# Kernel tuning notes

Measured on AMD Instinct MI355X. Metric: run time of the kernel, lower is better.

Reference implementation:

```python
import jax, jax.numpy as jnp
import numpy as np
from jax import lax

EMBED_DIM = 128
HIDDEN = 50
KS = 7
BN_EPS = 1e-5


def setup_inputs() -> dict:
    key = jax.random.key(0)
    ks = jax.random.split(key, 8)
    B, L, D, H = 4, 512, EMBED_DIM, HIDDEN
    x1 = jax.random.normal(ks[0], (B, L, D), jnp.float32)
    x2 = jax.random.normal(ks[1], (B, L, D), jnp.float32)
    # conv1 (1x1) weight stored as [H, 2D] (spatial dims of size 1 dropped)
    conv1_w = jax.random.normal(ks[2], (H, 2 * D), jnp.float32) * (1.0 / np.sqrt(2 * D))
    conv1_b = jnp.zeros((H,), jnp.float32)
    bn1_g = jnp.ones((H,), jnp.float32)
    bn1_b = jnp.zeros((H,), jnp.float32)
    w2 = jax.random.normal(ks[3], (1, H, KS, KS), jnp.float32) * (1.0 / np.sqrt(H * KS * KS))
    conv2_w = 0.5 * (w2 + jnp.swapaxes(w2, 2, 3))  # clip(): symmetrize kernel
    conv2_b = jnp.zeros((1,), jnp.float32)
    bn2_g = jnp.ones((1,), jnp.float32)
    bn2_b = jnp.zeros((1,), jnp.float32)
    return {"x1": x1, "x2": x2, "conv1_w": conv1_w, "conv1_b": conv1_b,
            "bn1_g": bn1_g, "bn1_b": bn1_b, "conv2_w": conv2_w, "conv2_b": conv2_b,
            "bn2_g": bn2_g, "bn2_b": bn2_b}


def _batch_norm(x, g, b):
    # train-mode BN: batch statistics over (N, H, W), biased variance (PyTorch)
    m = jnp.mean(x, axis=(0, 2, 3), keepdims=True)
    v = jnp.var(x, axis=(0, 2, 3), keepdims=True)
    xn = (x - m) * lax.rsqrt(v + BN_EPS)
    return xn * g[None, :, None, None] + b[None, :, None, None]


def reference(x1, x2, conv1_w, conv1_b, bn1_g, bn1_b, conv2_w, conv2_b, bn2_g, bn2_b):
    # x1, x2: [B, L, D] -> channel-first [B, D, L]
    x1c = jnp.swapaxes(x1, 1, 2)
    x2c = jnp.swapaxes(x2, 1, 2)
    D = x1c.shape[1]
    w_dif, w_mul = conv1_w[:, :D], conv1_w[:, D:]
    # 1x1 conv over concat([|x1_i - x2_j|, x1_i * x2_j]) fused as two contractions
    dif = jnp.abs(x1c[:, :, :, None] - x2c[:, :, None, :])        # [B, D, L1, L2]
    h = jnp.einsum('bdij,hd->bhij', dif, w_dif)
    h = h + jnp.einsum('bdi,bdj,hd->bhij', x1c, x2c, w_mul)       # mul term, no [B,D,L,L] materialized by hand
    h = h + conv1_b[None, :, None, None]
    h = jax.nn.relu(h)                 # activation1 BEFORE batch_norm1 (as in source)
    h = _batch_norm(h, bn1_g, bn1_b)
    # conv2: symmetric 7x7, padding ks//2 == SAME for odd ks
    y = lax.conv_general_dilated(h, conv2_w, window_strides=(1, 1), padding='SAME',
                                 dimension_numbers=('NCHW', 'OIHW', 'NCHW'))
    y = y + conv2_b[None, :, None, None]
    y = _batch_norm(y, bn2_g, bn2_b)
    y = jax.nn.sigmoid(y)
    return y[:, 0, :, :]               # squeeze channel -> [B, L1, L2]
```

## Files before the change

kernel.cpp:

```cpp
#include <hip/hip_runtime.h>

#define LL 512
#define DD 128
#define HH 50
#define JW 520

typedef short v8s __attribute__((ext_vector_type(8)));
typedef float f32x4 __attribute__((ext_vector_type(4)));
typedef unsigned int u32x4 __attribute__((ext_vector_type(4)));

__device__ __forceinline__ unsigned cvtpk(float a, float b) {
  unsigned r;
  asm("v_cvt_pk_bf16_f32 %0, %1, %2" : "=v"(r) : "v"(a), "v"(b));
  return r;
}
__device__ __forceinline__ unsigned cvtpkabs(float a, float b) {
  unsigned r;
  asm("v_cvt_pk_bf16_f32 %0, abs(%1), abs(%2)" : "=v"(r) : "v"(a), "v"(b));
  return r;
}
__device__ __forceinline__ unsigned short f2bf(float f) {
  unsigned u = __builtin_bit_cast(unsigned, f);
  u = (u + 0x7fffu + ((u >> 16) & 1u)) >> 16;
  return (unsigned short)u;
}
__device__ __forceinline__ void gload_lds16(const unsigned short* g, unsigned short* l) {
  __builtin_amdgcn_global_load_lds(
      (const __attribute__((address_space(1))) unsigned int*)g,
      (__attribute__((address_space(3))) unsigned int*)l, 16, 0, 0);
}

__global__ __launch_bounds__(256, 2) void pass1(
    const float* __restrict__ x1, const float* __restrict__ x2,
    const float* __restrict__ c1w, const float* __restrict__ c1b,
    unsigned short* __restrict__ hbuf, float* __restrict__ partials)
{
  __shared__ float x1s[32][128];
  __shared__ unsigned short wgt[64][264];
  __shared__ float stred[4][128];

  const int tid = threadIdx.x;
  const int wv = tid >> 6, lane = tid & 63;
  const int lh = lane & 15, lg = lane >> 4;
  const int bx = blockIdx.x, by = blockIdx.y, bz = blockIdx.z;
  const int j0 = bx << 6, i0 = by << 5;

  {
    int r = tid >> 3, c = (tid & 7) << 4;
    const float* g = x1 + ((size_t)(bz * LL + i0 + r) * DD + c);
#pragma unroll
    for (int u = 0; u < 4; ++u)
      *(f32x4*)&x1s[r][c + 4 * u] = *(const f32x4*)(g + 4 * u);
  }
  {
#pragma unroll
    for (int it = 0; it < 16; ++it) {
      int flat = (it * 256 + tid) << 2;
      int h = flat >> 8, col = flat & 255;
      f32x4 v = (h < HH) ? *(const f32x4*)(c1w + flat) : f32x4{0.f, 0.f, 0.f, 0.f};
      unsigned lo = cvtpk(v[0], v[1]), hi = cvtpk(v[2], v[3]);
      *(unsigned long long*)&wgt[h][col] = ((unsigned long long)hi << 32) | lo;
    }
  }
  __syncthreads();

  v8s bfr[4][8];
  {
    const unsigned wbase = (unsigned)(size_t)
        ((__attribute__((address_space(3))) char*)&wgt[0][0]);
#pragma unroll
    for (int n = 0; n < 4; n++)
#pragma unroll
      for (int kt = 0; kt < 8; kt++) {
        unsigned off = wbase + (unsigned)(((n * 16 + lh) * 264 + kt * 32 + lg * 8) << 1);
        asm volatile("ds_read_b128 %0, %1" : "=v"(bfr[n][kt]) : "v"(off));
      }
    asm volatile("s_waitcnt lgkmcnt(0)" ::: "memory");
    __builtin_amdgcn_sched_barrier(0);
  }

  float x2v[4][8];
  {
    const int j = j0 + (wv << 4) + lh;
    const float* g = x2 + ((size_t)(bz * LL + j) * DD + (lg << 3));
#pragma unroll
    for (int kt = 0; kt < 4; kt++) {
      f32x4 a = *(const f32x4*)(g + kt * 32);
      f32x4 b = *(const f32x4*)(g + kt * 32 + 4);
#pragma unroll
      for (int e = 0; e < 4; e++) { x2v[kt][e] = a[e]; x2v[kt][4 + e] = b[e]; }
    }
  }
  float bias[4][4];
#pragma unroll
  for (int n = 0; n < 4; n++)
#pragma unroll
    for (int q = 0; q < 4; q++) {
      int h = n * 16 + (lg << 2) + q;
      bias[n][q] = (h < HH) ? c1b[h] : 0.f;
    }

  float ssum[4][4], ssq[4][4];
#pragma unroll
  for (int n = 0; n < 4; n++)
#pragma unroll
    for (int q = 0; q < 4; q++) { ssum[n][q] = 0.f; ssq[n][q] = 0.f; }

  unsigned short* hb = hbuf +
      ((size_t)(bz * LL + i0) * JW + 4 + j0 + (wv << 4) + lh) * 64 + (lg << 2);

#pragma unroll 2
  for (int di = 0; di < 32; ++di) {
    f32x4 acc[4];
#pragma unroll
    for (int n = 0; n < 4; n++) acc[n] = f32x4{0.f, 0.f, 0.f, 0.f};
#pragma unroll
    for (int kt = 0; kt < 4; ++kt) {
      f32x4 p = *(const f32x4*)&x1s[di][kt * 32 + (lg << 3)];
      f32x4 r = *(const f32x4*)&x1s[di][kt * 32 + (lg << 3) + 4];
      float xv[8];
#pragma unroll
      for (int e = 0; e < 4; e++) { xv[e] = p[e]; xv[4 + e] = r[e]; }
      u32x4 ad, am;
#pragma unroll
      for (int m = 0; m < 4; m++) {
        ad[m] = cvtpkabs(xv[2*m] - x2v[kt][2*m], xv[2*m+1] - x2v[kt][2*m+1]);
        am[m] = cvtpk(xv[2*m] * x2v[kt][2*m], xv[2*m+1] * x2v[kt][2*m+1]);
      }
      v8s vad = __builtin_bit_cast(v8s, ad);
      v8s vam = __builtin_bit_cast(v8s, am);
#pragma unroll
      for (int n = 0; n < 4; n++)
        acc[n] = __builtin_amdgcn_mfma_f32_16x16x32_bf16(bfr[n][kt], vad, acc[n], 0, 0, 0);
#pragma unroll
      for (int n = 0; n < 4; n++)
        acc[n] = __builtin_amdgcn_mfma_f32_16x16x32_bf16(bfr[n][kt + 4], vam, acc[n], 0, 0, 0);
    }
    unsigned short* hp = hb + (size_t)di * (JW * 64);
#pragma unroll
    for (int n = 0; n < 4; ++n) {
      float vv[4];
#pragma unroll
      for (int q = 0; q < 4; ++q) {
        float v = acc[n][q] + bias[n][q];
        v = fmaxf(v, 0.f);
        ssum[n][q] += v; ssq[n][q] += v * v;
        vv[q] = v;
      }
      unsigned lo = cvtpk(vv[0], vv[1]), hi = cvtpk(vv[2], vv[3]);
      *(unsigned long long*)(hp + n * 16) = ((unsigned long long)hi << 32) | lo;
    }
  }

#pragma unroll
  for (int n = 0; n < 4; ++n)
#pragma unroll
    for (int q = 0; q < 4; ++q) {
      float s = ssum[n][q], t = ssq[n][q];
#pragma unroll
      for (int m = 1; m < 16; m <<= 1) { s += __shfl_xor(s, m); t += __shfl_xor(t, m); }
      if (lh == 0) {
        stred[wv][n * 16 + (lg << 2) + q] = s;
        stred[wv][64 + n * 16 + (lg << 2) + q] = t;
      }
    }
  __syncthreads();
  if (tid < 128) {
    int bid = (bz * gridDim.y + by) * gridDim.x + bx;
    partials[bid * 128 + tid] = stred[0][tid] + stred[1][tid] + stred[2][tid] + stred[3][tid];
  }

  if (bx == 0 || bx == 7) {
    const int jb = (bx == 0) ? 0 : 516;
#pragma unroll
    for (int k = 0; k < 4; ++k) {
      int unit = tid + (k << 8);
      int ii = unit >> 5;
      int rem = unit & 31;
      int jj = jb + (rem >> 3);
      int ch = (rem & 7) << 3;
      u32x4 z = {0u, 0u, 0u, 0u};
      *(u32x4*)&hbuf[((size_t)(bz * LL + i0 + ii) * JW + jj) * 64 + ch] = z;
    }
  }
}

__global__ void pass2a(const float* __restrict__ partials, float* __restrict__ red1)
{
  __shared__ float acc2[2][128];
  const int tid = threadIdx.x, b = blockIdx.x;
  const int slot = tid & 127, half = tid >> 7;
  float s = 0.f;
#pragma unroll
  for (int k = 0; k < 4; k++)
    s += partials[(b * 8 + half * 4 + k) * 128 + slot];
  acc2[half][slot] = s;
  __syncthreads();
  if (tid < 128) red1[b * 128 + tid] = acc2[0][tid] + acc2[1][tid];
}

__global__ void pass2b(const float* __restrict__ red1,
                       const float* __restrict__ c2w, const float* __restrict__ c2b,
                       const float* __restrict__ bn1g, const float* __restrict__ bn1b,
                       unsigned short* __restrict__ wA, float* __restrict__ tmap)
{
  __shared__ float acc2[2][128];
  __shared__ float sq[128];
  __shared__ float aa[64], cc[64];
  __shared__ float wlds[2450];
  __shared__ float tpart[49][5];
  const int tid = threadIdx.x;
  const int slot = tid & 127, half = tid >> 7;
  float s = 0.f;
#pragma unroll
  for (int k = 0; k < 32; k++) s += red1[(half * 32 + k) * 128 + slot];
  acc2[half][slot] = s;
  __syncthreads();
  if (tid < 128) sq[tid] = acc2[0][tid] + acc2[1][tid];
  for (int i = tid; i < 2450; i += 256) wlds[i] = c2w[i];
  __syncthreads();
  if (tid < HH) {
    float S = sq[tid], Q = sq[64 + tid];
    const float N = 4.0f * 512.f * 512.f;
    float m = S / N, v = fmaxf(Q / N - m * m, 0.f);
    float a = bn1g[tid] * rsqrtf(v + 1e-5f);
    aa[tid] = a;
    cc[tid] = bn1b[tid] - m * a;
  }
  __syncthreads();
  for (int idx = tid; idx < 16 * 448; idx += 256) {
    int ky = idx / 448, r = idx - ky * 448;
    int kx = r >> 6, ch = r & 63;
    float v = (ky < 7 && ch < HH) ? aa[ch] * wlds[ch * 49 + ky * 7 + kx] : 0.f;
    wA[idx] = f2bf(v);
  }
  if (tid < 245) {
    int c = tid / 5, g = tid - (tid / 5) * 5;
    int ci = c / 7, cj = c - (c / 7) * 7;
    int kylo = ci < 3 ? 3 - ci : 0, kyhi = ci > 3 ? 9 - ci : 6;
    int kxlo = cj < 3 ? 3 - cj : 0, kxhi = cj > 3 ? 9 - cj : 6;
    float t = 0.f;
    for (int h = g * 10; h < g * 10 + 10; h++) {
      float sm = 0.f;
      for (int ky = kylo; ky <= kyhi; ky++)
        for (int kx = kxlo; kx <= kxhi; kx++) sm += wlds[h * 49 + ky * 7 + kx];
      t += cc[h] * sm;
    }
    tpart[c][g] = t;
  }
  __syncthreads();
  if (tid < 49)
    tmap[tid] = c2b[0] + tpart[tid][0] + tpart[tid][1] + tpart[tid][2]
              + tpart[tid][3] + tpart[tid][4];
}

__global__ __launch_bounds__(256, 4) void pass3(
    const unsigned short* __restrict__ hbuf, const unsigned short* __restrict__ wA,
    const float* __restrict__ tmap, float* __restrict__ ybuf, float* __restrict__ part2)
{
  __shared__ unsigned short T[2][72 * 64];
  __shared__ float tm[49];
  __shared__ float rs[4], rq[4];

  const int tid = threadIdx.x;
  const int wv = tid >> 6, lane = tid & 63;
  const int lh = lane & 15, lg = lane >> 4;
  const int bx = blockIdx.x, by = blockIdx.y, bz = blockIdx.z;
  const int j0 = bx << 6, i0 = by << 4;

  v8s afr[14];
#pragma unroll
  for (int kt = 0; kt < 14; kt++)
    afr[kt] = *(const v8s*)&wA[lh * 448 + kt * 32 + (lg << 3)];

  if (tid < 49) tm[tid] = tmap[tid];

  const int jc = (wv << 4) + lh;
  float ya[4] = {0.f, 0.f, 0.f, 0.f};

  auto stage = [&](int buf, int row) {
    const unsigned short* rowp = hbuf + ((size_t)(bz * LL + row) * JW + j0) * 64;
#pragma unroll
    for (int cc2 = 0; cc2 < 2; ++cc2) {
      const int c = wv + (cc2 << 2);
      const int u = (c << 6) + lane;
      const int tj = u >> 3, oct = u & 7;
      gload_lds16(rowp + tj * 64 + ((oct ^ (tj & 7)) << 3), &T[buf][c << 9]);
    }
    if (wv == 0) {
      const int u = 512 + lane;
      const int tj = u >> 3, oct = u & 7;
      gload_lds16(rowp + tj * 64 + ((oct ^ (tj & 7)) << 3), &T[buf][8 << 9]);
    }
  };

  { const int r0 = i0 - 3; if (r0 >= 0) stage(0, r0); }
  __syncthreads();

  for (int rb = 0; rb < 24; rb += 8) {
#pragma unroll
    for (int u8 = 0; u8 < 8; ++u8) {
      const int rr = rb + u8;
      const int r = i0 - 3 + rr;
      const int cur = rr & 1;
      if (rr + 1 < 22) {
        const int rn = r + 1;
        if (rn >= 0 && rn < LL) stage(cur ^ 1, rn);
      }
      if (rr < 22 && r >= 0 && r < LL) {
        f32x4 a0 = {0.f, 0.f, 0.f, 0.f}, a1 = {0.f, 0.f, 0.f, 0.f};
#pragma unroll
        for (int kt = 0; kt < 14; ++kt) {
          const int kx = kt >> 1;
          const int t = jc + 1 + kx;
          const int sl = ((kt & 1) << 2) + lg;
          v8s b = *(const v8s*)&T[cur][(t << 6) + ((sl ^ (t & 7)) << 3)];
          if (kt & 1) a1 = __builtin_amdgcn_mfma_f32_16x16x32_bf16(afr[kt], b, a1, 0, 0, 0);
          else        a0 = __builtin_amdgcn_mfma_f32_16x16x32_bf16(afr[kt], b, a0, 0, 0, 0);
        }
        float zq[4];
#pragma unroll
        for (int q = 0; q < 4; ++q) zq[q] = a0[q] + a1[q];
#pragma unroll
        for (int ky = 0; ky < 7; ++ky) {
          float zz = __shfl(zq[ky & 3], ((ky >> 2) << 4) + lh, 64);
          const int idx = rr - ky;
          const bool ok = ((unsigned)idx < 16u) && ((idx >> 2) == lg);
          ya[(u8 - ky) & 3] += ok ? zz : 0.f;
        }
      }
      __syncthreads();
    }
  }

  float sa = 0.f, qa = 0.f;
  const int jj = j0 + jc;
  const int cj = jj < 3 ? jj : (jj > 508 ? jj - 505 : 3);
#pragma unroll
  for (int s = 0; s < 4; ++s) {
    const int i = i0 + (lg << 2) + s;
    const int ci = i < 3 ? i : (i > 508 ? i - 505 : 3);
    float v = ya[s] + tm[ci * 7 + cj];
    ybuf[(size_t)(bz * LL + i) * LL + jj] = v;
    sa += v; qa += v * v;
  }
#pragma unroll
  for (int m = 1; m < 64; m <<= 1) { sa += __shfl_xor(sa, m); qa += __shfl_xor(qa, m); }
  if (lane == 0) { rs[wv] = sa; rq[wv] = qa; }
  __syncthreads();
  if (tid == 0) {
    const int bid = (bz * gridDim.y + by) * gridDim.x + bx;
    part2[bid] = rs[0] + rs[1] + rs[2] + rs[3];
    part2[1024 + bid] = rq[0] + rq[1] + rq[2] + rq[3];
  }
}

__global__ void pass3b(const float* __restrict__ part2, float* __restrict__ stats2)
{
  __shared__ float rs[4], rq[4];
  const int tid = threadIdx.x;
  float s = 0.f, q = 0.f;
  for (int i = tid; i < 1024; i += 256) { s += part2[i]; q += part2[1024 + i]; }
#pragma unroll
  for (int m = 1; m < 64; m <<= 1) { s += __shfl_xor(s, m); q += __shfl_xor(q, m); }
  const int wave = tid >> 6, lane = tid & 63;
  if (lane == 0) { rs[wave] = s; rq[wave] = q; }
  __syncthreads();
  if (tid == 0) {
    float S = rs[0] + rs[1] + rs[2] + rs[3];
    float Q = rq[0] + rq[1] + rq[2] + rq[3];
    const float N = 4.0f * 512.f * 512.f;
    float m2 = S / N, v2 = fmaxf(Q / N - m2 * m2, 0.f);
    stats2[0] = m2;
    stats2[1] = rsqrtf(v2 + 1e-5f);
  }
}

__global__ void pass4(const float* __restrict__ y, const float* __restrict__ stats2,
                      const float* __restrict__ bn2g, const float* __restrict__ bn2b,
                      float* __restrict__ out)
{
  const int idx = blockIdx.x * 256 + threadIdx.x;
  const float m2 = stats2[0], inv = stats2[1];
  const float g = bn2g[0], b = bn2b[0];
  f32x4 v = ((const f32x4*)y)[idx];
  f32x4 r;
#pragma unroll
  for (int e = 0; e < 4; e++) {
    float xn = (v[e] - m2) * inv * g + b;
    r[e] = 1.f / (1.f + __expf(-xn));
  }
  ((f32x4*)out)[idx] = r;
}

extern "C" void kernel_launch(void* const* d_in, const int* in_sizes, int n_in,
                              void* d_out, int out_size, void* d_ws, size_t ws_size,
                              hipStream_t stream) {
  (void)in_sizes; (void)n_in; (void)out_size; (void)ws_size;
  const float* x1   = (const float*)d_in[0];
  const float* x2   = (const float*)d_in[1];
  const float* c1w  = (const float*)d_in[2];
  const float* c1b  = (const float*)d_in[3];
  const float* bn1g = (const float*)d_in[4];
  const float* bn1b = (const float*)d_in[5];
  const float* c2w  = (const float*)d_in[6];
  const float* c2b  = (const float*)d_in[7];
  const float* bn2g = (const float*)d_in[8];
  const float* bn2b = (const float*)d_in[9];

  char* ws = (char*)d_ws;
  float* partials       = (float*)(ws + 0);
  float* red1           = (float*)(ws + 524288);
  float* part2          = (float*)(ws + 557056);
  unsigned short* wA    = (unsigned short*)(ws + 565248);
  float* tmap           = (float*)(ws + 579584);
  float* stats2         = (float*)(ws + 579840);
  float* ybuf           = (float*)(ws + 1048576);
  unsigned short* hbuf  = (unsigned short*)(ws + 5242880);

  pass1<<<dim3(8, 16, 4), 256, 0, stream>>>(x1, x2, c1w, c1b, hbuf, partials);
  pass2a<<<64, 256, 0, stream>>>(partials, red1);
  pass2b<<<1, 256, 0, stream>>>(red1, c2w, c2b, bn1g, bn1b, wA, tmap);
  pass3<<<dim3(8, 32, 4), 256, 0, stream>>>(hbuf, wA, tmap, ybuf, part2);
  pass3b<<<1, 256, 0, stream>>>(part2, stats2);
  pass4<<<1024, 256, 0, stream>>>(ybuf, stats2, bn2g, bn2b, (float*)d_out);
}
```

Before: 120.9 us.

## Pre-convert conv1 weights in a separate pass and stage pass1 inputs via direct-to-LDS loads

Adds a small pass0 kernel that converts conv1 weights to bf16 once, so each pass1 block no longer converts them itself. pass1 then loads the weights and its x1 tile straight into LDS with global_load_lds and drops the padded weight layout. It also packs the elementwise math into float2 operations and reuses the x1 buffer for the statistics reduction to cut LDS use. Separately, pass3 launch bounds drop from 4 to 3 blocks per SIMD. The costs are an extra kernel launch and possible LDS bank conflicts on the now-unpadded weight rows.

```diff
diff --git a/kernel.cpp b/kernel.cpp
--- a/kernel.cpp
+++ b/kernel.cpp
@@ -7,6 +7,7 @@
 
 typedef short v8s __attribute__((ext_vector_type(8)));
 typedef float f32x4 __attribute__((ext_vector_type(4)));
+typedef float f32x2 __attribute__((ext_vector_type(2)));
 typedef unsigned int u32x4 __attribute__((ext_vector_type(4)));
 
 __device__ __forceinline__ unsigned cvtpk(float a, float b) {
@@ -24,20 +25,26 @@
   u = (u + 0x7fffu + ((u >> 16) & 1u)) >> 16;
   return (unsigned short)u;
 }
-__device__ __forceinline__ void gload_lds16(const unsigned short* g, unsigned short* l) {
+__device__ __forceinline__ void gload16(const void* g, void* l) {
   __builtin_amdgcn_global_load_lds(
       (const __attribute__((address_space(1))) unsigned int*)g,
       (__attribute__((address_space(3))) unsigned int*)l, 16, 0, 0);
 }
 
+__global__ void pass0(const float* __restrict__ c1w, unsigned short* __restrict__ wbuf)
+{
+  const int idx = blockIdx.x * 256 + threadIdx.x;
+  const int r = idx >> 8;
+  wbuf[idx] = f2bf((r < HH) ? c1w[idx] : 0.f);
+}
+
 __global__ __launch_bounds__(256, 2) void pass1(
     const float* __restrict__ x1, const float* __restrict__ x2,
-    const float* __restrict__ c1w, const float* __restrict__ c1b,
+    const unsigned short* __restrict__ wbuf, const float* __restrict__ c1b,
     unsigned short* __restrict__ hbuf, float* __restrict__ partials)
 {
-  __shared__ float x1s[32][128];
-  __shared__ unsigned short wgt[64][264];
-  __shared__ float stred[4][128];
+  __shared__ unsigned short wlin[64 * 256];
+  __shared__ float x1s[32 * 128];
 
   const int tid = threadIdx.x;
   const int wv = tid >> 6, lane = tid & 63;
@@ -45,66 +52,60 @@
   const int bx = blockIdx.x, by = blockIdx.y, bz = blockIdx.z;
   const int j0 = bx << 6, i0 = by << 5;
 
+#pragma unroll
+  for (int k = 0; k < 8; ++k)
+    gload16(wbuf + (((k << 8) + tid) << 3), wlin + ((((k << 2) + wv) << 6) << 3));
   {
-    int r = tid >> 3, c = (tid & 7) << 4;
-    const float* g = x1 + ((size_t)(bz * LL + i0 + r) * DD + c);
-#pragma unroll
-    for (int u = 0; u < 4; ++u)
-      *(f32x4*)&x1s[r][c + 4 * u] = *(const f32x4*)(g + 4 * u);
-  }
-  {
-#pragma unroll
-    for (int it = 0; it < 16; ++it) {
-      int flat = (it * 256 + tid) << 2;
-      int h = flat >> 8, col = flat & 255;
-      f32x4 v = (h < HH) ? *(const f32x4*)(c1w + flat) : f32x4{0.f, 0.f, 0.f, 0.f};
-      unsigned lo = cvtpk(v[0], v[1]), hi = cvtpk(v[2], v[3]);
-      *(unsigned long long*)&wgt[h][col] = ((unsigned long long)hi << 32) | lo;
-    }
+    const float* x1base = x1 + (size_t)(bz * LL + i0) * DD;
+#pragma unroll
+    for (int k = 0; k < 4; ++k)
+      gload16(x1base + (((k << 8) + tid) << 2), x1s + ((((k << 2) + wv) << 6) << 2));
   }
   __syncthreads();
 
   v8s bfr[4][8];
   {
     const unsigned wbase = (unsigned)(size_t)
-        ((__attribute__((address_space(3))) char*)&wgt[0][0]);
+        ((__attribute__((address_space(3))) char*)&wlin[0]);
 #pragma unroll
     for (int n = 0; n < 4; n++)
 #pragma unroll
       for (int kt = 0; kt < 8; kt++) {
-        unsigned off = wbase + (unsigned)(((n * 16 + lh) * 264 + kt * 32 + lg * 8) << 1);
+        unsigned off = wbase + (unsigned)((((n * 16 + lh) << 8) + kt * 32 + lg * 8) << 1);
         asm volatile("ds_read_b128 %0, %1" : "=v"(bfr[n][kt]) : "v"(off));
       }
     asm volatile("s_waitcnt lgkmcnt(0)" ::: "memory");
     __builtin_amdgcn_sched_barrier(0);
   }
 
-  float x2v[4][8];
+  f32x2 x2p[4][4];
   {
     const int j = j0 + (wv << 4) + lh;
     const float* g = x2 + ((size_t)(bz * LL + j) * DD + (lg << 3));
 #pragma unroll
-    for (int kt = 0; kt < 4; kt++) {
-      f32x4 a = *(const f32x4*)(g + kt * 32);
-      f32x4 b = *(const f32x4*)(g + kt * 32 + 4);
-#pragma unroll
-      for (int e = 0; e < 4; e++) { x2v[kt][e] = a[e]; x2v[kt][4 + e] = b[e]; }
-    }
-  }
-  float bias[4][4];
+    for (int kt = 0; kt < 4; kt++)
+#pragma unroll
+      for (int m = 0; m < 4; m++)
+        x2p[kt][m] = *(const f32x2*)(g + kt * 32 + 2 * m);
+  }
+  f32x2 bias2[4][2];
 #pragma unroll
   for (int n = 0; n < 4; n++)
 #pragma unroll
-    for (int q = 0; q < 4; q++) {
-      int h = n * 16 + (lg << 2) + q;
-      bias[n][q] = (h < HH) ? c1b[h] : 0.f;
-    }
-
-  float ssum[4][4], ssq[4][4];
+    for (int h2 = 0; h2 < 2; h2++) {
+      int h0 = n * 16 + (lg << 2) + 2 * h2;
+      bias2[n][h2] = f32x2{(h0 < HH) ? c1b[h0] : 0.f,
+                           (h0 + 1 < HH) ? c1b[h0 + 1] : 0.f};
+    }
+
+  f32x2 ssum2[4][2], ssq2[4][2];
 #pragma unroll
   for (int n = 0; n < 4; n++)
 #pragma unroll
-    for (int q = 0; q < 4; q++) { ssum[n][q] = 0.f; ssq[n][q] = 0.f; }
+    for (int h2 = 0; h2 < 2; h2++) {
+      ssum2[n][h2] = f32x2{0.f, 0.f};
+      ssq2[n][h2] = f32x2{0.f, 0.f};
+    }
 
   unsigned short* hb = hbuf +
       ((size_t)(bz * LL + i0) * JW + 4 + j0 + (wv << 4) + lh) * 64 + (lg << 2);
@@ -116,16 +117,15 @@
     for (int n = 0; n < 4; n++) acc[n] = f32x4{0.f, 0.f, 0.f, 0.f};
 #pragma unroll
     for (int kt = 0; kt < 4; ++kt) {
-      f32x4 p = *(const f32x4*)&x1s[di][kt * 32 + (lg << 3)];
-      f32x4 r = *(const f32x4*)&x1s[di][kt * 32 + (lg << 3) + 4];
-      float xv[8];
-#pragma unroll
-      for (int e = 0; e < 4; e++) { xv[e] = p[e]; xv[4 + e] = r[e]; }
+      const float* xr = &x1s[(di << 7) + kt * 32 + (lg << 3)];
       u32x4 ad, am;
 #pragma unroll
       for (int m = 0; m < 4; m++) {
-        ad[m] = cvtpkabs(xv[2*m] - x2v[kt][2*m], xv[2*m+1] - x2v[kt][2*m+1]);
-        am[m] = cvtpk(xv[2*m] * x2v[kt][2*m], xv[2*m+1] * x2v[kt][2*m+1]);
+        f32x2 xp = *(const f32x2*)(xr + 2 * m);
+        f32x2 d = xp - x2p[kt][m];
+        f32x2 pr = xp * x2p[kt][m];
+        ad[m] = cvtpkabs(d[0], d[1]);
+        am[m] = cvtpk(pr[0], pr[1]);
       }
       v8s vad = __builtin_bit_cast(v8s, ad);
       v8s vam = __builtin_bit_cast(v8s, am);
@@ -139,35 +139,35 @@
     unsigned short* hp = hb + (size_t)di * (JW * 64);
 #pragma unroll
     for (int n = 0; n < 4; ++n) {
-      float vv[4];
-#pragma unroll
-      for (int q = 0; q < 4; ++q) {
-        float v = acc[n][q] + bias[n][q];
-        v = fmaxf(v, 0.f);
-        ssum[n][q] += v; ssq[n][q] += v * v;
-        vv[q] = v;
-      }
-      unsigned lo = cvtpk(vv[0], vv[1]), hi = cvtpk(vv[2], vv[3]);
+      f32x2 v0 = f32x2{acc[n][0], acc[n][1]} + bias2[n][0];
+      f32x2 v1 = f32x2{acc[n][2], acc[n][3]} + bias2[n][1];
+      v0 = __builtin_elementwise_max(v0, f32x2{0.f, 0.f});
+      v1 = __builtin_elementwise_max(v1, f32x2{0.f, 0.f});
+      ssum2[n][0] += v0; ssum2[n][1] += v1;
+      ssq2[n][0] += v0 * v0; ssq2[n][1] += v1 * v1;
+      unsigned lo = cvtpk(v0[0], v0[1]), hi = cvtpk(v1[0], v1[1]);
       *(unsigned long long*)(hp + n * 16) = ((unsigned long long)hi << 32) | lo;
     }
   }
 
+  __syncthreads();
+  float* stred = x1s;
 #pragma unroll
   for (int n = 0; n < 4; ++n)
 #pragma unroll
     for (int q = 0; q < 4; ++q) {
-      float s = ssum[n][q], t = ssq[n][q];
+      float s = ssum2[n][q >> 1][q & 1], t = ssq2[n][q >> 1][q & 1];
 #pragma unroll
       for (int m = 1; m < 16; m <<= 1) { s += __shfl_xor(s, m); t += __shfl_xor(t, m); }
       if (lh == 0) {
-        stred[wv][n * 16 + (lg << 2) + q] = s;
-        stred[wv][64 + n * 16 + (lg << 2) + q] = t;
+        stred[(wv << 7) + n * 16 + (lg << 2) + q] = s;
+        stred[(wv << 7) + 64 + n * 16 + (lg << 2) + q] = t;
       }
     }
   __syncthreads();
   if (tid < 128) {
     int bid = (bz * gridDim.y + by) * gridDim.x + bx;
-    partials[bid * 128 + tid] = stred[0][tid] + stred[1][tid] + stred[2][tid] + stred[3][tid];
+    partials[bid * 128 + tid] = stred[tid] + stred[128 + tid] + stred[256 + tid] + stred[384 + tid];
   }
 
   if (bx == 0 || bx == 7) {
@@ -254,7 +254,7 @@
               + tpart[tid][3] + tpart[tid][4];
 }
 
-__global__ __launch_bounds__(256, 4) void pass3(
+__global__ __launch_bounds__(256, 3) void pass3(
     const unsigned short* __restrict__ hbuf, const unsigned short* __restrict__ wA,
     const float* __restrict__ tmap, float* __restrict__ ybuf, float* __restrict__ part2)
 {
@@ -285,12 +285,12 @@
       const int c = wv + (cc2 << 2);
       const int u = (c << 6) + lane;
       const int tj = u >> 3, oct = u & 7;
-      gload_lds16(rowp + tj * 64 + ((oct ^ (tj & 7)) << 3), &T[buf][c << 9]);
+      gload16(rowp + tj * 64 + ((oct ^ (tj & 7)) << 3), &T[buf][c << 9]);
     }
     if (wv == 0) {
       const int u = 512 + lane;
       const int tj = u >> 3, oct = u & 7;
-      gload_lds16(rowp + tj * 64 + ((oct ^ (tj & 7)) << 3), &T[buf][8 << 9]);
+      gload16(rowp + tj * 64 + ((oct ^ (tj & 7)) << 3), &T[buf][8 << 9]);
     }
   };
 
@@ -415,10 +415,12 @@
   unsigned short* wA    = (unsigned short*)(ws + 565248);
   float* tmap           = (float*)(ws + 579584);
   float* stats2         = (float*)(ws + 579840);
+  unsigned short* wbuf  = (unsigned short*)(ws + 581632);
   float* ybuf           = (float*)(ws + 1048576);
   unsigned short* hbuf  = (unsigned short*)(ws + 5242880);
 
-  pass1<<<dim3(8, 16, 4), 256, 0, stream>>>(x1, x2, c1w, c1b, hbuf, partials);
+  pass0<<<64, 256, 0, stream>>>(c1w, wbuf);
+  pass1<<<dim3(8, 16, 4), 256, 0, stream>>>(x1, x2, wbuf, c1b, hbuf, partials);
   pass2a<<<64, 256, 0, stream>>>(partials, red1);
   pass2b<<<1, 256, 0, stream>>>(red1, c2w, c2b, bn1g, bn1b, wA, tmap);
   pass3<<<dim3(8, 32, 4), 256, 0, stream>>>(hbuf, wA, tmap, ybuf, part2);
```

Result: slower. 126.0 us (+4.2%).
